# Kernel optimization log

Measured on AMD Instinct MI355X. Metric: run time of the kernel, lower is better.

Reference implementation:

```python
import jax, jax.numpy as jnp
import numpy as np
from jax import lax

B, T, DE, DT = 64, 511, 400, 100
D = DE + DT              # encoder + tag embedding concat
S = T + 1                # head sentinel prepended
HG, HE, M = 384, 64, 32  # graph hidden, edge hidden, band width


def lstm_layer(x, h0, c0, Wih, Whh, bih, bhh):
    """x: [N, L, in] -> [N, L, H]; torch LSTM gate order (i, f, g, o)."""
    def step(carry, xt):
        h, c = carry
        gates = xt @ Wih.T + bih + h @ Whh.T + bhh
        i, f, g, o = jnp.split(gates, 4, axis=-1)
        c = jax.nn.sigmoid(f) * c + jax.nn.sigmoid(i) * jnp.tanh(g)
        h = jax.nn.sigmoid(o) * jnp.tanh(c)
        return (h, c), h
    _, ys = lax.scan(step, (h0, c0), jnp.swapaxes(x, 0, 1))
    return jnp.swapaxes(ys, 0, 1)


def setup_inputs() -> dict:
    key = jax.random.key(0)
    ks = jax.random.split(key, 32)
    def u(k, shape, h):
        s = 1.0 / np.sqrt(h)
        return jax.random.uniform(k, shape, jnp.float32, -s, s)
    return {
        "input": jax.random.normal(ks[0], (B, T, DE), jnp.float32),
        "tag_embeddings": jax.random.normal(ks[1], (B, T, DT), jnp.float32),
        "mask": jnp.ones((B, T), jnp.int32),
        "head_indices": jax.random.randint(ks[2], (B, T), 0, S),
        "head_sentinel": jax.random.normal(ks[3], (D,), jnp.float32),
        "bos_past": jnp.zeros((1,), jnp.float32),
        # graph LSTM (2 layers, dropout inactive at eval)
        "g_Wih0": u(ks[4], (4 * HG, D), HG),  "g_Whh0": u(ks[5], (4 * HG, HG), HG),
        "g_bih0": u(ks[6], (4 * HG,), HG),     "g_bhh0": u(ks[7], (4 * HG,), HG),
        "g_Wih1": u(ks[8], (4 * HG, HG), HG),  "g_Whh1": u(ks[9], (4 * HG, HG), HG),
        "g_bih1": u(ks[10], (4 * HG,), HG),    "g_bhh1": u(ks[11], (4 * HG,), HG),
        # edge LSTM past (2 layers, input size 1)
        "e_Wih0": u(ks[12], (4 * HE, 1), HE),  "e_Whh0": u(ks[13], (4 * HE, HE), HE),
        "e_bih0": u(ks[14], (4 * HE,), HE),    "e_bhh0": u(ks[15], (4 * HE,), HE),
        "e_Wih1": u(ks[16], (4 * HE, HE), HE), "e_Whh1": u(ks[17], (4 * HE, HE), HE),
        "e_bih1": u(ks[18], (4 * HE,), HE),    "e_bhh1": u(ks[19], (4 * HE,), HE),
        "g2e_W": u(ks[20], (HE, HG), HG),      "g2e_b": u(ks[21], (HE,), HG),
        "cls_W": u(ks[22], (1, HE), HE),       "cls_b": u(ks[23], (1,), HE),
        "ht_W": u(ks[24], (DT, HG), HG),       "ht_b": u(ks[25], (DT,), HG),
        "dt_W": u(ks[26], (DT, HG), HG),       "dt_b": u(ks[27], (DT,), HG),
    }


def reference(input, tag_embeddings, mask, head_indices, head_sentinel, bos_past,
              g_Wih0, g_Whh0, g_bih0, g_bhh0, g_Wih1, g_Whh1, g_bih1, g_bhh1,
              e_Wih0, e_Whh0, e_bih0, e_bhh0, e_Wih1, e_Whh1, e_bih1, e_bhh1,
              g2e_W, g2e_b, cls_W, cls_b, ht_W, ht_b, dt_W, dt_b):
    # --- sentinel prepend + adjust_for_sentinel ---
    x = jnp.concatenate([input, tag_embeddings], axis=-1)                      # [B,T,D]
    x = jnp.concatenate([jnp.broadcast_to(head_sentinel, (B, 1, D)), x], 1)    # [B,S,D]
    mask_s = jnp.concatenate([jnp.ones((B, 1), mask.dtype), mask], axis=1)
    heads = jnp.concatenate([jnp.zeros((B, 1), head_indices.dtype), head_indices], axis=1)
    # --- packed graph LSTM (2 layers, zero init); pad_packed zeros masked positions ---
    zg = jnp.zeros((B, HG), x.dtype)
    h = lstm_layer(x, zg, zg, g_Wih0, g_Whh0, g_bih0, g_bhh0)
    graph_state = lstm_layer(h, zg, zg, g_Wih1, g_Whh1, g_bih1, g_bhh1)        # [B,S,HG]
    graph_state = graph_state * mask_s[..., None].astype(graph_state.dtype)
    # --- edge_pass_train (split=False): teacher-forced banded edge LSTM ---
    proj = graph_state.reshape(B * S, HG) @ g2e_W.T + g2e_b                    # [B*S,HE]
    Lm = min(M, S)
    A_sq = jax.nn.one_hot(heads, S, dtype=jnp.float32)                         # adj_indices_to_adj_matrix
    A_in = A_sq[:, :, :Lm].reshape(B * S, Lm, 1)                               # make_adj_sequence band
    bos = jnp.broadcast_to(bos_past.reshape(1, 1, 1), (B * S, 1, 1))
    A_in = jnp.concatenate([bos, A_in], axis=1)                                # [B*S,Lm+1,1]
    ze = jnp.zeros((B * S, HE), proj.dtype)
    e = lstm_layer(A_in, proj, ze, e_Wih0, e_Whh0, e_bih0, e_bhh0)             # h0=proj per layer, c0=0
    e = lstm_layer(e, proj, ze, e_Wih1, e_Whh1, e_bih1, e_bhh1)
    edge_logits = e @ cls_W.T + cls_b                                          # [B*S,Lm+1,1]
    Ap = edge_logits[:, 1:, 0].reshape(B, S, Lm)                               # drop bos step
    # banded writeback: arc_logits[:, i, :min(S,M)] = Ap[:, i, :] for every i
    arc_logits = jnp.zeros((B, S, S), graph_state.dtype).at[:, :, :Lm].set(Ap)
    # --- tag feedforwards (dropout = identity at eval) ---
    head_tag = jax.nn.elu(graph_state @ ht_W.T + ht_b)
    dep_tag = jax.nn.elu(graph_state @ dt_W.T + dt_b)
    return arc_logits, head_tag, dep_tag
```

## Files before the change

kernel.cpp:

```cpp
#include <hip/hip_runtime.h>
#include <hip/hip_bf16.h>
#include <stdint.h>

#define BB   64
#define TT   511
#define SS   512
#define DD   500
#define KXP  512
#define HG   384
#define G4   1536
#define HE   64
#define E4   256
#define NSEQ (BB*SS)

typedef __hip_bfloat16 bf16;
typedef float  floatx4 __attribute__((ext_vector_type(4)));
typedef int    intx4   __attribute__((ext_vector_type(4)));
typedef __bf16 bfrag8  __attribute__((ext_vector_type(8)));

static __device__ __forceinline__ floatx4 MFMA16(bfrag8 a, bfrag8 b, floatx4 c){
  return __builtin_amdgcn_mfma_f32_16x16x32_bf16(a, b, c, 0, 0, 0);
}
static __device__ __forceinline__ float sigm_(float x){ return 1.f/(1.f + __expf(-x)); }
static __device__ __forceinline__ float tanh_(float x){
  x = fminf(fmaxf(x, -15.f), 15.f);
  float e = __expf(2.f*x);
  return (e - 1.f)/(e + 1.f);
}
static __device__ __forceinline__ float actv(float x, bool isg){
  float s = 1.f/(1.f + __expf(isg ? -2.f*x : -x));
  return isg ? (2.f*s - 1.f) : s;
}
static __device__ __forceinline__ float b2f(unsigned short u){
  union { unsigned int i; float f; } x; x.i = ((unsigned int)u)<<16; return x.f;
}
static __device__ __forceinline__ unsigned short f2bu(float f){
  bf16 b = __float2bfloat16(f);
  return *reinterpret_cast<unsigned short*>(&b);
}
static __device__ __forceinline__ bfrag8 asfrag(intx4 v){
  union { intx4 i; bfrag8 f; } u; u.i = v; return u.f;
}

static __device__ __forceinline__ bfrag8 ldfrag_coh(const bf16* p){
  unsigned long long u0 = __hip_atomic_load((const unsigned long long*)p,     __ATOMIC_RELAXED, __HIP_MEMORY_SCOPE_SYSTEM);
  unsigned long long u1 = __hip_atomic_load((const unsigned long long*)p + 1, __ATOMIC_RELAXED, __HIP_MEMORY_SCOPE_SYSTEM);
  union { unsigned long long u[2]; bfrag8 f; } x; x.u[0]=u0; x.u[1]=u1;
  return x.f;
}
static __device__ __forceinline__ void stpair_coh(bf16* p, float lo, float hi){
  unsigned int pk = (unsigned int)f2bu(lo) | ((unsigned int)f2bu(hi) << 16);
  __hip_atomic_store((unsigned int*)p, pk, __ATOMIC_RELAXED, __HIP_MEMORY_SCOPE_SYSTEM);
}
static __device__ __forceinline__ void pollge(unsigned int* p, unsigned int tgt){
  while (__hip_atomic_load(p, __ATOMIC_RELAXED, __HIP_MEMORY_SCOPE_AGENT) < tgt)
    __builtin_amdgcn_s_sleep(4);
}

__global__ __launch_bounds__(256) void prep_x(const float* __restrict__ input,
    const float* __restrict__ tag, const float* __restrict__ sent,
    bf16* __restrict__ Xb)
{
  const size_t stp = (size_t)gridDim.x * blockDim.x;
  for (size_t i = (size_t)blockIdx.x*blockDim.x + threadIdx.x; i < (size_t)NSEQ*KXP; i += stp){
    int m = (int)(i >> 9), k = (int)(i & 511);
    int b = m >> 9, s = m & 511;
    float v;
    if (k >= DD)        v = 0.f;
    else if (s == 0)    v = sent[k];
    else if (k < 400)   v = input[(size_t)(b*TT + s-1)*400 + k];
    else                v = tag  [(size_t)(b*TT + s-1)*100 + (k-400)];
    Xb[i] = __float2bfloat16(v);
  }
}

__global__ __launch_bounds__(256) void prep_w(
  const float* __restrict__ gWih0, const float* __restrict__ gWhh0,
  const float* __restrict__ gbih0, const float* __restrict__ gbhh0,
  const float* __restrict__ gWih1, const float* __restrict__ gWhh1,
  const float* __restrict__ gbih1, const float* __restrict__ gbhh1,
  const float* __restrict__ eWih0, const float* __restrict__ eWhh0,
  const float* __restrict__ ebih0, const float* __restrict__ ebhh0,
  const float* __restrict__ eWih1, const float* __restrict__ eWhh1,
  const float* __restrict__ ebih1, const float* __restrict__ ebhh1,
  const float* __restrict__ g2eW, const float* __restrict__ htW, const float* __restrict__ dtW,
  bf16* __restrict__ W0i, bf16* __restrict__ W0r, bf16* __restrict__ W1c,
  float* __restrict__ gb0, float* __restrict__ gb1,
  bf16* __restrict__ eW0b, bf16* __restrict__ eW1ab, bf16* __restrict__ eW1bb,
  float* __restrict__ eb0, float* __restrict__ eb1, float* __restrict__ ew0cv,
  bf16* __restrict__ g2eWb, bf16* __restrict__ htWb, bf16* __restrict__ dtWb)
{
  const int st = blockIdx.x*blockDim.x + threadIdx.x;
  const int gs = gridDim.x*blockDim.x;
  for (int i=st; i<G4*KXP; i+=gs){ int n=i>>9, k=i&511; int j=n>>2, g=n&3;
      W0i[i] = __float2bfloat16(k<DD ? gWih0[(size_t)(g*HG+j)*DD+k] : 0.f); }
  for (int i=st; i<G4*HG; i+=gs){ int n=i/HG, k=i-n*HG; int j=n>>2, g=n&3;
      W0r[i] = __float2bfloat16(gWhh0[(size_t)(g*HG+j)*HG+k]); }
  for (int i=st; i<G4*768; i+=gs){ int n=i/768, k=i-n*768; int j=n>>2, g=n&3;
      W1c[i] = __float2bfloat16(k<HG ? gWih1[(size_t)(g*HG+j)*HG+k]
                                     : gWhh1[(size_t)(g*HG+j)*HG+(k-HG)]); }
  for (int i=st; i<G4; i+=gs){ int j=i>>2, g=i&3; int s=g*HG+j;
      gb0[i]=gbih0[s]+gbhh0[s]; gb1[i]=gbih1[s]+gbhh1[s]; }
  for (int i=st; i<E4*HE; i+=gs){ eW0b[i]=__float2bfloat16(eWhh0[i]);
      eW1ab[i]=__float2bfloat16(eWih1[i]); eW1bb[i]=__float2bfloat16(eWhh1[i]); }
  for (int i=st; i<E4; i+=gs){ eb0[i]=ebih0[i]+ebhh0[i]; eb1[i]=ebih1[i]+ebhh1[i];
      ew0cv[i]=eWih0[i]; }
  for (int i=st; i<HE*HG; i+=gs) g2eWb[i]=__float2bfloat16(g2eW[i]);
  for (int i=st; i<128*HG; i+=gs){
      htWb[i] = __float2bfloat16(i<100*HG ? htW[i] : 0.f);
      dtWb[i] = __float2bfloat16(i<100*HG ? dtW[i] : 0.f); }
}

template<int KTOT,int BN,int WAVES_M,int WAVES_N,int EPI>
__global__ __launch_bounds__(256) void gemm_mfma(
    const bf16* __restrict__ A, const bf16* __restrict__ Wt,
    const float* __restrict__ bias, const int* __restrict__ mask,
    void* __restrict__ outp, int Nreal)
{
  constexpr int WMT = 128/(WAVES_M*16);
  constexpr int WNT = BN /(WAVES_N*16);
  __shared__ alignas(16) bf16 As[128][32];
  __shared__ alignas(16) bf16 Bs[BN][32];
  const int tid = threadIdx.x;
  const int bm = blockIdx.x & 255, bn = blockIdx.x >> 8;
  const int m0 = bm*128, n0 = bn*BN;
  const int wid = tid>>6, l = tid&63, lj = l&15, lq = l>>4;
  const int wm = wid / WAVES_N, wn = wid % WAVES_N;
  floatx4 acc[WMT][WNT] = {};
  for (int k0 = 0; k0 < KTOT; k0 += 32){
    __syncthreads();
    for (int c = tid; c < 128*4; c += 256){
      int row = c>>2, ch = c&3;
      *(uint4*)&As[row][ch*8] = *(const uint4*)&A[(size_t)(m0+row)*KTOT + k0 + ch*8];
    }
    for (int c = tid; c < BN*4; c += 256){
      int row = c>>2, ch = c&3;
      *(uint4*)&Bs[row][ch*8] = *(const uint4*)&Wt[(size_t)(n0+row)*KTOT + k0 + ch*8];
    }
    __syncthreads();
    bfrag8 af[WMT]; bfrag8 bfr[WNT];
    #pragma unroll
    for (int mi=0;mi<WMT;++mi) af[mi]  = *(const bfrag8*)&As[wm*WMT*16 + mi*16 + lj][lq*8];
    #pragma unroll
    for (int ni=0;ni<WNT;++ni) bfr[ni] = *(const bfrag8*)&Bs[wn*WNT*16 + ni*16 + lj][lq*8];
    #pragma unroll
    for (int mi=0;mi<WMT;++mi)
      #pragma unroll
      for (int ni=0;ni<WNT;++ni)
        acc[mi][ni] = MFMA16(af[mi], bfr[ni], acc[mi][ni]);
  }
  #pragma unroll
  for (int mi=0;mi<WMT;++mi){
    #pragma unroll
    for (int ni=0;ni<WNT;++ni){
      #pragma unroll
      for (int r=0;r<4;++r){
        int grow = m0 + wm*WMT*16 + mi*16 + 4*lq + r;
        int gcol = n0 + wn*WNT*16 + ni*16 + lj;
        float v = acc[mi][ni][r];
        if (EPI == 0){
          v += bias[gcol];
          ((bf16*)outp)[(size_t)grow*Nreal + gcol] = __float2bfloat16(v);
        } else if (EPI == 3){
          v += bias[gcol];
          int s = grow & 511, b = grow >> 9;
          ((bf16*)outp)[((size_t)s*BB + b)*G4 + gcol] = __float2bfloat16(v);
        } else {
          int s = grow & 511, b = grow >> 9;
          float mk = (s==0) ? 1.f : (float)mask[b*TT + s - 1];
          v = v*mk + bias[gcol];
          if (EPI == 1){
            ((bf16*)outp)[(size_t)grow*Nreal + gcol] = __float2bfloat16(v);
          } else {
            v = v > 0.f ? v : expm1f(v);
            if (gcol < Nreal) ((float*)outp)[(size_t)grow*Nreal + gcol] = v;
          }
        }
      }
    }
  }
}

template<int IS1>
__device__ __forceinline__ void rnn_body(int bid, int tid,
    const bf16* __restrict__ G0t, const bf16* __restrict__ Wsrc,
    const float* __restrict__ gb1,
    bf16* __restrict__ h0r, bf16* __restrict__ h1seq, unsigned int* __restrict__ flags)
{
  constexpr int KW = IS1 ? 768 : 384;
  constexpr int KF = IS1 ? 24 : 12;
  const int bl = IS1 ? bid-48 : bid;
  const int w = tid>>6, l = tid&63, lj = l&15, lq = l>>4;
  const int m0 = w*16;
  const int n0 = bl*32;
  const int a  = lj>>2;
  const int gl = l&3;
  const bool isg = (gl==2);

  intx4 Wr0[KF], Wr1[KF];
  #pragma unroll
  for (int kf=0; kf<KF; ++kf){
    Wr0[kf] = *(const intx4*)&Wsrc[(size_t)(n0 + lj)*KW      + kf*32 + lq*8];
    Wr1[kf] = *(const intx4*)&Wsrc[(size_t)(n0 + 16 + lj)*KW + kf*32 + lq*8];
  }
  #pragma unroll
  for (int kf=0; kf<KF; ++kf)
    asm volatile("" : "+v"(Wr0[kf]), "+v"(Wr1[kf]));

  float bi0 = 0.f, bi1 = 0.f;
  if (IS1){ bi0 = gb1[n0 + 4*a + gl]; bi1 = gb1[n0 + 16 + 4*a + gl]; }

  float c0s[4]={0,0,0,0}, c1s[4]={0,0,0,0};
  unsigned short g0pre[2][4];
  if (!IS1){
    #pragma unroll
    for (int nt=0;nt<2;++nt)
      #pragma unroll
      for (int r=0;r<4;++r)
        g0pre[nt][r] = *(const unsigned short*)&G0t[(size_t)(m0 + 4*lq + r)*G4 + n0 + nt*16 + 4*a + gl];
  }
  const int ITMAX = IS1 ? SS : (SS-1);
  for (int it=0; it<=ITMAX; ++it){
    if (it > 0){
      if (tid < 48){
        pollge(&flags[(size_t)tid*16], (unsigned)it);
      } else if (tid < 96){
        if (IS1){ if (it >= 2) pollge(&flags[(size_t)tid*16], (unsigned)it); }
        else    { if (it >= 3) pollge(&flags[(size_t)tid*16], (unsigned)(it-2)); }
      }
      __syncthreads();
    }
    if (!IS1 || it >= 1){
      const int t = IS1 ? it-1 : it;
      bfrag8 ha[KF];
      if (IS1){
        const bf16* hb0 = h0r + (size_t)((it-1)&3)*(BB*HG) + (size_t)(m0+lj)*HG;
        #pragma unroll
        for (int kf=0;kf<12;++kf) ha[kf] = ldfrag_coh(hb0 + kf*32 + lq*8);
        if (t > 0){
          const bf16* hb1 = h1seq + ((size_t)(m0+lj)*SS + (t-1))*HG;
          #pragma unroll
          for (int kf=12;kf<24;++kf) ha[kf] = ldfrag_coh(hb1 + (kf-12)*32 + lq*8);
        }
      } else if (t > 0){
        const bf16* hb = h0r + (size_t)((t-1)&3)*(BB*HG) + (size_t)(m0+lj)*HG;
        #pragma unroll
        for (int kf=0;kf<12;++kf) ha[kf] = ldfrag_coh(hb + kf*32 + lq*8);
      }
      floatx4 aA0={0,0,0,0}, aB0={0,0,0,0}, aA1={0,0,0,0}, aB1={0,0,0,0};
      if (IS1 || t > 0){
        #pragma unroll
        for (int kf=0;kf<12;++kf){
          if (kf&1){ aB0 = MFMA16(ha[kf], asfrag(Wr0[kf]), aB0); aB1 = MFMA16(ha[kf], asfrag(Wr1[kf]), aB1); }
          else     { aA0 = MFMA16(ha[kf], asfrag(Wr0[kf]), aA0); aA1 = MFMA16(ha[kf], asfrag(Wr1[kf]), aA1); }
        }
      }
      if (IS1 && t > 0){
        #pragma unroll
        for (int kf=12;kf<24;++kf){
          if (kf&1){ aB0 = MFMA16(ha[kf], asfrag(Wr0[kf]), aB0); aB1 = MFMA16(ha[kf], asfrag(Wr1[kf]), aB1); }
          else     { aA0 = MFMA16(ha[kf], asfrag(Wr0[kf]), aA0); aA1 = MFMA16(ha[kf], asfrag(Wr1[kf]), aA1); }
        }
      }
      const floatx4 s0 = aA0 + aB0, s1 = aA1 + aB1;
      #pragma unroll
      for (int nt=0; nt<2; ++nt){
        #pragma unroll
        for (int r=0; r<4; ++r){
          float x = nt ? s1[r] : s0[r];
          x += IS1 ? (nt ? bi1 : bi0) : b2f(g0pre[nt][r]);
          float av = actv(x, isg);
          float i_ = __shfl(av, (l&60)|0);
          float f_ = __shfl(av, (l&60)|1);
          float g_ = __shfl(av, (l&60)|2);
          float o_ = __shfl(av, (l&60)|3);
          float cp = nt ? c1s[r] : c0s[r];
          float c = f_*cp + i_*g_;
          if (nt) c1s[r] = c; else c0s[r] = c;
          float h = o_*tanh_(c);
          float hn = __shfl(h, l^4);
          if ((l&7) == 0){
            int bb = m0 + 4*lq + r;
            int jh = bl*8 + nt*4 + a;
            bf16* hp = IS1 ? (h1seq + ((size_t)bb*SS + t)*HG + jh)
                           : (h0r + (size_t)(it&3)*(BB*HG) + (size_t)bb*HG + jh);
            stpair_coh(hp, h, hn);
          }
        }
      }
      if (!IS1 && it+1 < SS){
        #pragma unroll
        for (int nt=0;nt<2;++nt)
          #pragma unroll
          for (int r=0;r<4;++r)
            g0pre[nt][r] = *(const unsigned short*)&G0t[((size_t)(it+1)*BB + m0 + 4*lq + r)*G4 + n0 + nt*16 + 4*a + gl];
      }
    }
    asm volatile("s_waitcnt vmcnt(0) lgkmcnt(0)" ::: "memory");
    __syncthreads();
    if (tid == 0)
      __hip_atomic_store(&flags[(size_t)bid*16], (unsigned)(it+1),
                         __ATOMIC_RELAXED, __HIP_MEMORY_SCOPE_AGENT);
  }
}

__global__ __launch_bounds__(256,1) void graph_rnn(
    const bf16* __restrict__ G0t, const bf16* __restrict__ W0r, const bf16* __restrict__ W1c,
    const float* __restrict__ gb1, bf16* __restrict__ h0r, bf16* __restrict__ h1seq,
    unsigned int* flags)
{
  if (blockIdx.x < 48) rnn_body<0>(blockIdx.x, threadIdx.x, G0t, W0r, gb1, h0r, h1seq, flags);
  else                 rnn_body<1>(blockIdx.x, threadIdx.x, G0t, W1c, gb1, h0r, h1seq, flags);
}

__global__ __launch_bounds__(256) void edge_lstm(
    const bf16* __restrict__ projb,
    const bf16* __restrict__ eW0b, const bf16* __restrict__ eW1ab, const bf16* __restrict__ eW1bb,
    const float* __restrict__ eb0, const float* __restrict__ eb1, const float* __restrict__ ew0c,
    const float* __restrict__ clsW, const float* __restrict__ clsb_p, const float* __restrict__ bos_p,
    const int* __restrict__ heads, float* __restrict__ arc)
{
  __shared__ alignas(16) bf16 hbuf0[16][72];
  __shared__ alignas(16) bf16 hbuf1[16][72];
  __shared__ float lbuf[4][16];
  const int tid = threadIdx.x, w = tid>>6, l = tid&63, lj = l&15, lq = l>>4;
  const int seq0 = blockIdx.x * 16;
  const int jglob = w*16 + lj;
  for (int i = tid; i < 16*64; i += 256){
    int sl = i >> 6, jj = i & 63;
    bf16 v = projb[(size_t)(seq0+sl)*HE + jj];
    hbuf0[sl][jj] = v; hbuf1[sl][jj] = v;
  }
  bfrag8 W0f[4][2], W1af[4][2], W1bf[4][2];
  #pragma unroll
  for (int g=0; g<4; ++g){
    #pragma unroll
    for (int kk=0; kk<2; ++kk){
      size_t offw = (size_t)(g*HE + jglob)*HE + kk*32 + lq*8;
      W0f [g][kk] = *(const bfrag8*)&eW0b [offw];
      W1af[g][kk] = *(const bfrag8*)&eW1ab[offw];
      W1bf[g][kk] = *(const bfrag8*)&eW1bb[offw];
    }
  }
  float ebr0[4], ebr1[4], ewr[4];
  #pragma unroll
  for (int g=0; g<4; ++g){ ebr0[g]=eb0[g*HE+jglob]; ebr1[g]=eb1[g*HE+jglob]; ewr[g]=ew0c[g*HE+jglob]; }
  const float clswj = clsW[jglob];
  const float bos = bos_p[0], clsb = clsb_p[0];
  int hd[4]; float c0r[4]={0,0,0,0}, c1r[4]={0,0,0,0};
  #pragma unroll
  for (int r=0;r<4;++r){
    int sq = seq0 + 4*lq + r;
    int b = sq >> 9, s = sq & 511;
    hd[r] = (s==0) ? 0 : heads[b*TT + s - 1];
  }
  __syncthreads();
  for (int j=0; j<33; ++j){
    floatx4 acc0[4] = {};
    bfrag8 a0[2];
    #pragma unroll
    for (int kk=0; kk<2; ++kk)
      a0[kk] = *(const bfrag8*)((const char*)&hbuf0[0][0] + lj*144 + kk*64 + lq*16);
    #pragma unroll
    for (int g=0; g<4; ++g)
      #pragma unroll
      for (int kk=0; kk<2; ++kk)
        acc0[g] = MFMA16(a0[kk], W0f[g][kk], acc0[g]);
    __syncthreads();
    float h0v[4];
    #pragma unroll
    for (int r=0;r<4;++r){
      float x = (j==0) ? bos : ((hd[r] == j-1) ? 1.f : 0.f);
      float pi = acc0[0][r] + ebr0[0] + x*ewr[0];
      float pf = acc0[1][r] + ebr0[1] + x*ewr[1];
      float pg = acc0[2][r] + ebr0[2] + x*ewr[2];
      float po = acc0[3][r] + ebr0[3] + x*ewr[3];
      float i_=sigm_(pi), f_=sigm_(pf), g_=tanh_(pg), o_=sigm_(po);
      c0r[r] = f_*c0r[r] + i_*g_;
      h0v[r] = o_*tanh_(c0r[r]);
    }
    #pragma unroll
    for (int r=0;r<4;++r) hbuf0[4*lq + r][jglob] = __float2bfloat16(h0v[r]);
    __syncthreads();
    floatx4 acc1[4] = {};
    bfrag8 a1[2], a2[2];
    #pragma unroll
    for (int kk=0;kk<2;++kk){
      a1[kk] = *(const bfrag8*)((const char*)&hbuf0[0][0] + lj*144 + kk*64 + lq*16);
      a2[kk] = *(const bfrag8*)((const char*)&hbuf1[0][0] + lj*144 + kk*64 + lq*16);
    }
    #pragma unroll
    for (int g=0; g<4; ++g){
      #pragma unroll
      for (int kk=0;kk<2;++kk){
        acc1[g] = MFMA16(a1[kk], W1af[g][kk], acc1[g]);
        acc1[g] = MFMA16(a2[kk], W1bf[g][kk], acc1[g]);
      }
    }
    __syncthreads();
    float p[4];
    #pragma unroll
    for (int r=0;r<4;++r){
      float pi = acc1[0][r] + ebr1[0];
      float pf = acc1[1][r] + ebr1[1];
      float pg = acc1[2][r] + ebr1[2];
      float po = acc1[3][r] + ebr1[3];
      float i_=sigm_(pi), f_=sigm_(pf), g_=tanh_(pg), o_=sigm_(po);
      c1r[r] = f_*c1r[r] + i_*g_;
      float h1 = o_*tanh_(c1r[r]);
      hbuf1[4*lq + r][jglob] = __float2bfloat16(h1);
      p[r] = h1 * clswj;
    }
    #pragma unroll
    for (int mk=1; mk<16; mk<<=1)
      #pragma unroll
      for (int r=0;r<4;++r) p[r] += __shfl_xor(p[r], mk, 64);
    if (lj == 0){
      #pragma unroll
      for (int r=0;r<4;++r) lbuf[w][4*lq + r] = p[r];
    }
    __syncthreads();
    if (tid < 16 && j >= 1){
      int sq = seq0 + tid;
      float v = lbuf[0][tid] + lbuf[1][tid] + lbuf[2][tid] + lbuf[3][tid] + clsb;
      arc[(size_t)sq*SS + (j-1)] = v;
    }
  }
}

extern "C" void kernel_launch(void* const* d_in, const int* in_sizes, int n_in,
                              void* d_out, int out_size, void* d_ws, size_t ws_size,
                              hipStream_t stream)
{
  const float* input = (const float*)d_in[0];
  const float* tag   = (const float*)d_in[1];
  const int*   mask  = (const int*)  d_in[2];
  const int*   heads = (const int*)  d_in[3];
  const float* sent  = (const float*)d_in[4];
  const float* bosp  = (const float*)d_in[5];
  const float* gWih0 = (const float*)d_in[6];
  const float* gWhh0 = (const float*)d_in[7];
  const float* gbih0 = (const float*)d_in[8];
  const float* gbhh0 = (const float*)d_in[9];
  const float* gWih1 = (const float*)d_in[10];
  const float* gWhh1 = (const float*)d_in[11];
  const float* gbih1 = (const float*)d_in[12];
  const float* gbhh1 = (const float*)d_in[13];
  const float* eWih0 = (const float*)d_in[14];
  const float* eWhh0 = (const float*)d_in[15];
  const float* ebih0 = (const float*)d_in[16];
  const float* ebhh0 = (const float*)d_in[17];
  const float* eWih1 = (const float*)d_in[18];
  const float* eWhh1 = (const float*)d_in[19];
  const float* ebih1 = (const float*)d_in[20];
  const float* ebhh1 = (const float*)d_in[21];
  const float* g2eW  = (const float*)d_in[22];
  const float* g2eb  = (const float*)d_in[23];
  const float* clsW  = (const float*)d_in[24];
  const float* clsb  = (const float*)d_in[25];
  const float* htW   = (const float*)d_in[26];
  const float* htb   = (const float*)d_in[27];
  const float* dtW   = (const float*)d_in[28];
  const float* dtb   = (const float*)d_in[29];

  char* wsb = (char*)d_ws;
  size_t off = 0;
  auto take = [&](size_t bytes)->char* {
    char* p = wsb + off;
    off = (off + bytes + 255) & ~(size_t)255;
    return p;
  };
  bf16*  Xb     = (bf16*) take((size_t)NSEQ*KXP*2);
  bf16*  W0i    = (bf16*) take((size_t)G4*KXP*2);
  bf16*  W0r    = (bf16*) take((size_t)G4*HG*2);
  bf16*  W1c    = (bf16*) take((size_t)G4*768*2);
  float* gb0i   = (float*)take(G4*4);
  float* gb1i   = (float*)take(G4*4);
  bf16*  G0t    = (bf16*) take((size_t)NSEQ*G4*2);
  bf16*  h0ring = (bf16*) take((size_t)4*BB*HG*2);
  bf16*  h1seq  = (bf16*) take((size_t)NSEQ*HG*2);
  unsigned int* flags = (unsigned int*)take(96*16*4);
  bf16*  projb  = (bf16*) take((size_t)NSEQ*HE*2);
  bf16*  eW0b   = (bf16*) take(E4*HE*2);
  bf16*  eW1ab  = (bf16*) take(E4*HE*2);
  bf16*  eW1bb  = (bf16*) take(E4*HE*2);
  float* eb0w   = (float*)take(E4*4);
  float* eb1w   = (float*)take(E4*4);
  float* ew0cw  = (float*)take(E4*4);
  bf16*  g2eWb  = (bf16*) take(HE*HG*2);
  bf16*  htWb   = (bf16*) take(128*HG*2);
  bf16*  dtWb   = (bf16*) take(128*HG*2);

  (void)hipMemsetAsync(d_out, 0, (size_t)16777216*4, stream);
  (void)hipMemsetAsync(flags, 0, 96*16*4, stream);

  prep_x<<<2048,256,0,stream>>>(input, tag, sent, Xb);
  prep_w<<<512,256,0,stream>>>(gWih0,gWhh0,gbih0,gbhh0,gWih1,gWhh1,gbih1,gbhh1,
                               eWih0,eWhh0,ebih0,ebhh0,eWih1,eWhh1,ebih1,ebhh1,
                               g2eW,htW,dtW,
                               W0i,W0r,W1c,gb0i,gb1i,eW0b,eW1ab,eW1bb,
                               eb0w,eb1w,ew0cw,g2eWb,htWb,dtWb);

  gemm_mfma<KXP,128,2,2,3><<<3072,256,0,stream>>>(Xb, W0i, gb0i, nullptr, (void*)G0t, G4);

  graph_rnn<<<96,256,0,stream>>>(G0t, W0r, W1c, gb1i, h0ring, h1seq, flags);

  gemm_mfma<HG,64,4,1,1><<<256,256,0,stream>>>(h1seq, g2eWb, g2eb, mask, (void*)projb, HE);

  edge_lstm<<<2048,256,0,stream>>>(projb, eW0b, eW1ab, eW1bb, eb0w, eb1w, ew0cw,
                                   clsW, clsb, bosp, heads, (float*)d_out);

  gemm_mfma<HG,128,2,2,2><<<256,256,0,stream>>>(h1seq, htWb, htb, mask,
      (void*)((float*)d_out + 16777216), 100);
  gemm_mfma<HG,128,2,2,2><<<256,256,0,stream>>>(h1seq, dtWb, dtb, mask,
      (void*)((float*)d_out + 16777216 + 3276800), 100);
}
```

Baseline: 4.934 ms.

## Replace per-step flag barriers with poison-sentinel dataflow sync in graph RNN

```diff
diff --git a/kernel.cpp b/kernel.cpp
--- a/kernel.cpp
+++ b/kernel.cpp
@@ -12,6 +12,8 @@
 #define HE   64
 #define E4   256
 #define NSEQ (BB*SS)
+#define NRING 32
+#define POISON32 0x7FC07FC0u
 
 typedef __hip_bfloat16 bf16;
 typedef float  floatx4 __attribute__((ext_vector_type(4)));
@@ -42,19 +44,22 @@
   union { intx4 i; bfrag8 f; } u; u.i = v; return u.f;
 }
 
-static __device__ __forceinline__ bfrag8 ldfrag_coh(const bf16* p){
+static __device__ __forceinline__ intx4 ld16_chk(const bf16* p){
   unsigned long long u0 = __hip_atomic_load((const unsigned long long*)p,     __ATOMIC_RELAXED, __HIP_MEMORY_SCOPE_SYSTEM);
   unsigned long long u1 = __hip_atomic_load((const unsigned long long*)p + 1, __ATOMIC_RELAXED, __HIP_MEMORY_SCOPE_SYSTEM);
-  union { unsigned long long u[2]; bfrag8 f; } x; x.u[0]=u0; x.u[1]=u1;
-  return x.f;
+  union { unsigned long long u[2]; intx4 v; } x; x.u[0]=u0; x.u[1]=u1;
+  return x.v;
+}
+static __device__ __forceinline__ bool okfrag(intx4 v){
+  return (((unsigned)v.x) != POISON32) & (((unsigned)v.y) != POISON32) &
+         (((unsigned)v.z) != POISON32) & (((unsigned)v.w) != POISON32);
 }
 static __device__ __forceinline__ void stpair_coh(bf16* p, float lo, float hi){
   unsigned int pk = (unsigned int)f2bu(lo) | ((unsigned int)f2bu(hi) << 16);
   __hip_atomic_store((unsigned int*)p, pk, __ATOMIC_RELAXED, __HIP_MEMORY_SCOPE_SYSTEM);
 }
-static __device__ __forceinline__ void pollge(unsigned int* p, unsigned int tgt){
-  while (__hip_atomic_load(p, __ATOMIC_RELAXED, __HIP_MEMORY_SCOPE_AGENT) < tgt)
-    __builtin_amdgcn_s_sleep(4);
+static __device__ __forceinline__ void st_poison(bf16* p){
+  __hip_atomic_store((unsigned int*)p, POISON32, __ATOMIC_RELAXED, __HIP_MEMORY_SCOPE_SYSTEM);
 }
 
 __global__ __launch_bounds__(256) void prep_x(const float* __restrict__ input,
@@ -88,7 +93,8 @@
   float* __restrict__ gb0, float* __restrict__ gb1,
   bf16* __restrict__ eW0b, bf16* __restrict__ eW1ab, bf16* __restrict__ eW1bb,
   float* __restrict__ eb0, float* __restrict__ eb1, float* __restrict__ ew0cv,
-  bf16* __restrict__ g2eWb, bf16* __restrict__ htWb, bf16* __restrict__ dtWb)
+  bf16* __restrict__ g2eWb, bf16* __restrict__ htWb, bf16* __restrict__ dtWb,
+  unsigned int* __restrict__ ring_u, unsigned int* __restrict__ h1_u)
 {
   const int st = blockIdx.x*blockDim.x + threadIdx.x;
   const int gs = gridDim.x*blockDim.x;
@@ -109,6 +115,8 @@
   for (int i=st; i<128*HG; i+=gs){
       htWb[i] = __float2bfloat16(i<100*HG ? htW[i] : 0.f);
       dtWb[i] = __float2bfloat16(i<100*HG ? dtW[i] : 0.f); }
+  for (int i=st; i<NRING*BB*HG/2; i+=gs) ring_u[i] = POISON32;
+  for (int i=st; i<NSEQ*HG/2;     i+=gs) h1_u[i]   = POISON32;
 }
 
 template<int KTOT,int BN,int WAVES_M,int WAVES_N,int EPI>
@@ -221,45 +229,64 @@
   }
   const int ITMAX = IS1 ? SS : (SS-1);
   for (int it=0; it<=ITMAX; ++it){
-    if (it > 0){
-      if (tid < 48){
-        pollge(&flags[(size_t)tid*16], (unsigned)it);
-      } else if (tid < 96){
-        if (IS1){ if (it >= 2) pollge(&flags[(size_t)tid*16], (unsigned)it); }
-        else    { if (it >= 3) pollge(&flags[(size_t)tid*16], (unsigned)(it-2)); }
-      }
-      __syncthreads();
+    if (!IS1 && (it&7)==0 && it>=16){
+      const unsigned tgt = (unsigned)(it-8);
+      while (true){
+        unsigned f0 = __hip_atomic_load(&flags[(size_t)(l)*16],     __ATOMIC_RELAXED, __HIP_MEMORY_SCOPE_AGENT);
+        unsigned f1 = __hip_atomic_load(&flags[(size_t)(l+64)*16],  __ATOMIC_RELAXED, __HIP_MEMORY_SCOPE_AGENT);
+        unsigned f2 = __hip_atomic_load(&flags[(size_t)(l+128)*16], __ATOMIC_RELAXED, __HIP_MEMORY_SCOPE_AGENT);
+        if (__all(f0>=tgt && f1>=tgt && f2>=tgt)) break;
+        __builtin_amdgcn_s_sleep(16);
+      }
     }
     if (!IS1 || it >= 1){
       const int t = IS1 ? it-1 : it;
-      bfrag8 ha[KF];
+      intx4 ha[KF];
       if (IS1){
-        const bf16* hb0 = h0r + (size_t)((it-1)&3)*(BB*HG) + (size_t)(m0+lj)*HG;
-        #pragma unroll
-        for (int kf=0;kf<12;++kf) ha[kf] = ldfrag_coh(hb0 + kf*32 + lq*8);
+        const bf16* hb0 = h0r + (size_t)((it-1)&(NRING-1))*(BB*HG) + (size_t)(m0+lj)*HG;
         if (t > 0){
           const bf16* hb1 = h1seq + ((size_t)(m0+lj)*SS + (t-1))*HG;
-          #pragma unroll
-          for (int kf=12;kf<24;++kf) ha[kf] = ldfrag_coh(hb1 + (kf-12)*32 + lq*8);
+          while (true){
+            bool ok = true;
+            #pragma unroll
+            for (int kf=0;kf<12;++kf){ ha[kf] = ld16_chk(hb0 + kf*32 + lq*8); ok &= okfrag(ha[kf]); }
+            #pragma unroll
+            for (int kf=12;kf<24;++kf){ ha[kf] = ld16_chk(hb1 + (kf-12)*32 + lq*8); ok &= okfrag(ha[kf]); }
+            if (__all(ok)) break;
+            __builtin_amdgcn_s_sleep(1);
+          }
+        } else {
+          while (true){
+            bool ok = true;
+            #pragma unroll
+            for (int kf=0;kf<12;++kf){ ha[kf] = ld16_chk(hb0 + kf*32 + lq*8); ok &= okfrag(ha[kf]); }
+            if (__all(ok)) break;
+            __builtin_amdgcn_s_sleep(1);
+          }
         }
       } else if (t > 0){
-        const bf16* hb = h0r + (size_t)((t-1)&3)*(BB*HG) + (size_t)(m0+lj)*HG;
-        #pragma unroll
-        for (int kf=0;kf<12;++kf) ha[kf] = ldfrag_coh(hb + kf*32 + lq*8);
+        const bf16* hb = h0r + (size_t)((t-1)&(NRING-1))*(BB*HG) + (size_t)(m0+lj)*HG;
+        while (true){
+          bool ok = true;
+          #pragma unroll
+          for (int kf=0;kf<12;++kf){ ha[kf] = ld16_chk(hb + kf*32 + lq*8); ok &= okfrag(ha[kf]); }
+          if (__all(ok)) break;
+          __builtin_amdgcn_s_sleep(1);
+        }
       }
       floatx4 aA0={0,0,0,0}, aB0={0,0,0,0}, aA1={0,0,0,0}, aB1={0,0,0,0};
       if (IS1 || t > 0){
         #pragma unroll
         for (int kf=0;kf<12;++kf){
-          if (kf&1){ aB0 = MFMA16(ha[kf], asfrag(Wr0[kf]), aB0); aB1 = MFMA16(ha[kf], asfrag(Wr1[kf]), aB1); }
-          else     { aA0 = MFMA16(ha[kf], asfrag(Wr0[kf]), aA0); aA1 = MFMA16(ha[kf], asfrag(Wr1[kf]), aA1); }
+          if (kf&1){ aB0 = MFMA16(asfrag(ha[kf]), asfrag(Wr0[kf]), aB0); aB1 = MFMA16(asfrag(ha[kf]), asfrag(Wr1[kf]), aB1); }
+          else     { aA0 = MFMA16(asfrag(ha[kf]), asfrag(Wr0[kf]), aA0); aA1 = MFMA16(asfrag(ha[kf]), asfrag(Wr1[kf]), aA1); }
         }
       }
       if (IS1 && t > 0){
         #pragma unroll
         for (int kf=12;kf<24;++kf){
-          if (kf&1){ aB0 = MFMA16(ha[kf], asfrag(Wr0[kf]), aB0); aB1 = MFMA16(ha[kf], asfrag(Wr1[kf]), aB1); }
-          else     { aA0 = MFMA16(ha[kf], asfrag(Wr0[kf]), aA0); aA1 = MFMA16(ha[kf], asfrag(Wr1[kf]), aA1); }
+          if (kf&1){ aB0 = MFMA16(asfrag(ha[kf]), asfrag(Wr0[kf]), aB0); aB1 = MFMA16(asfrag(ha[kf]), asfrag(Wr1[kf]), aB1); }
+          else     { aA0 = MFMA16(asfrag(ha[kf]), asfrag(Wr0[kf]), aA0); aA1 = MFMA16(asfrag(ha[kf]), asfrag(Wr1[kf]), aA1); }
         }
       }
       const floatx4 s0 = aA0 + aB0, s1 = aA1 + aB1;
@@ -283,10 +310,21 @@
             int bb = m0 + 4*lq + r;
             int jh = bl*8 + nt*4 + a;
             bf16* hp = IS1 ? (h1seq + ((size_t)bb*SS + t)*HG + jh)
-                           : (h0r + (size_t)(it&3)*(BB*HG) + (size_t)bb*HG + jh);
+                           : (h0r + (size_t)(it&(NRING-1))*(BB*HG) + (size_t)bb*HG + jh);
             stpair_coh(hp, h, hn);
           }
         }
+      }
+      if (!IS1 && (l&7) == 0){
+        bf16* ps = h0r + (size_t)((it+8)&(NRING-1))*(BB*HG);
+        #pragma unroll
+        for (int nt=0;nt<2;++nt)
+          #pragma unroll
+          for (int r=0;r<4;++r){
+            int bb = m0 + 4*lq + r;
+            int jh = bl*8 + nt*4 + a;
+            st_poison(ps + (size_t)bb*HG + jh);
+          }
       }
       if (!IS1 && it+1 < SS){
         #pragma unroll
@@ -296,10 +334,8 @@
             g0pre[nt][r] = *(const unsigned short*)&G0t[((size_t)(it+1)*BB + m0 + 4*lq + r)*G4 + n0 + nt*16 + 4*a + gl];
       }
     }
-    asm volatile("s_waitcnt vmcnt(0) lgkmcnt(0)" ::: "memory");
-    __syncthreads();
-    if (tid == 0)
-      __hip_atomic_store(&flags[(size_t)bid*16], (unsigned)(it+1),
+    if (IS1 && l == 0)
+      __hip_atomic_store(&flags[(size_t)(bl*4 + w)*16], (unsigned)(it+1),
                          __ATOMIC_RELAXED, __HIP_MEMORY_SCOPE_AGENT);
   }
 }
@@ -477,9 +513,9 @@
   float* gb0i   = (float*)take(G4*4);
   float* gb1i   = (float*)take(G4*4);
   bf16*  G0t    = (bf16*) take((size_t)NSEQ*G4*2);
-  bf16*  h0ring = (bf16*) take((size_t)4*BB*HG*2);
+  bf16*  h0ring = (bf16*) take((size_t)NRING*BB*HG*2);
   bf16*  h1seq  = (bf16*) take((size_t)NSEQ*HG*2);
-  unsigned int* flags = (unsigned int*)take(96*16*4);
+  unsigned int* flags = (unsigned int*)take(192*16*4);
   bf16*  projb  = (bf16*) take((size_t)NSEQ*HE*2);
   bf16*  eW0b   = (bf16*) take(E4*HE*2);
   bf16*  eW1ab  = (bf16*) take(E4*HE*2);
@@ -492,14 +528,15 @@
   bf16*  dtWb   = (bf16*) take(128*HG*2);
 
   (void)hipMemsetAsync(d_out, 0, (size_t)16777216*4, stream);
-  (void)hipMemsetAsync(flags, 0, 96*16*4, stream);
+  (void)hipMemsetAsync(flags, 0, 192*16*4, stream);
 
   prep_x<<<2048,256,0,stream>>>(input, tag, sent, Xb);
   prep_w<<<512,256,0,stream>>>(gWih0,gWhh0,gbih0,gbhh0,gWih1,gWhh1,gbih1,gbhh1,
                                eWih0,eWhh0,ebih0,ebhh0,eWih1,eWhh1,ebih1,ebhh1,
                                g2eW,htW,dtW,
                                W0i,W0r,W1c,gb0i,gb1i,eW0b,eW1ab,eW1bb,
-                               eb0w,eb1w,ew0cw,g2eWb,htWb,dtWb);
+                               eb0w,eb1w,ew0cw,g2eWb,htWb,dtWb,
+                               (unsigned int*)h0ring, (unsigned int*)h1seq);
 
   gemm_mfma<KXP,128,2,2,3><<<3072,256,0,stream>>>(Xb, W0i, gb0i, nullptr, (void*)G0t, G4);
 
```

Result: slower. 7.380 ms (+49.6%).

## Replace block-level barriers with per-wave flags in persistent graph LSTM

Applied to the files above, without the earlier changes.

```diff
diff --git a/kernel.cpp b/kernel.cpp
--- a/kernel.cpp
+++ b/kernel.cpp
@@ -51,10 +51,6 @@
 static __device__ __forceinline__ void stpair_coh(bf16* p, float lo, float hi){
   unsigned int pk = (unsigned int)f2bu(lo) | ((unsigned int)f2bu(hi) << 16);
   __hip_atomic_store((unsigned int*)p, pk, __ATOMIC_RELAXED, __HIP_MEMORY_SCOPE_SYSTEM);
-}
-static __device__ __forceinline__ void pollge(unsigned int* p, unsigned int tgt){
-  while (__hip_atomic_load(p, __ATOMIC_RELAXED, __HIP_MEMORY_SCOPE_AGENT) < tgt)
-    __builtin_amdgcn_s_sleep(4);
 }
 
 __global__ __launch_bounds__(256) void prep_x(const float* __restrict__ input,
@@ -185,7 +181,7 @@
 __device__ __forceinline__ void rnn_body(int bid, int tid,
     const bf16* __restrict__ G0t, const bf16* __restrict__ Wsrc,
     const float* __restrict__ gb1,
-    bf16* __restrict__ h0r, bf16* __restrict__ h1seq, unsigned int* __restrict__ flags)
+    bf16* __restrict__ h0seq, bf16* __restrict__ h1seq, unsigned int* __restrict__ flags)
 {
   constexpr int KW = IS1 ? 768 : 384;
   constexpr int KF = IS1 ? 24 : 12;
@@ -219,22 +215,35 @@
       for (int r=0;r<4;++r)
         g0pre[nt][r] = *(const unsigned short*)&G0t[(size_t)(m0 + 4*lq + r)*G4 + n0 + nt*16 + 4*a + gl];
   }
+  unsigned int* myflag = flags + (size_t)(((IS1?48:0) + bl)*4 + w)*16;
+  unsigned int* f0p = flags + (size_t)((l)*4 + w)*16;
+  unsigned int* f1p = flags + (size_t)((48 + l)*4 + w)*16;
+
   const int ITMAX = IS1 ? SS : (SS-1);
   for (int it=0; it<=ITMAX; ++it){
-    if (it > 0){
-      if (tid < 48){
-        pollge(&flags[(size_t)tid*16], (unsigned)it);
-      } else if (tid < 96){
-        if (IS1){ if (it >= 2) pollge(&flags[(size_t)tid*16], (unsigned)it); }
-        else    { if (it >= 3) pollge(&flags[(size_t)tid*16], (unsigned)(it-2)); }
-      }
-      __syncthreads();
+    if (it >= 1){
+      const unsigned tgt = (unsigned)it;
+      const bool need = (l < 48);
+      while (true){
+        bool ok = true;
+        if (need){
+          unsigned f0 = __hip_atomic_load(f0p, __ATOMIC_RELAXED, __HIP_MEMORY_SCOPE_AGENT);
+          ok = (f0 >= tgt);
+          if (IS1){
+            unsigned f1 = __hip_atomic_load(f1p, __ATOMIC_RELAXED, __HIP_MEMORY_SCOPE_AGENT);
+            ok = ok && (f1 >= tgt);
+          }
+        }
+        if (__all(ok)) break;
+        __builtin_amdgcn_s_sleep(1);
+      }
+      asm volatile("" ::: "memory");
     }
     if (!IS1 || it >= 1){
       const int t = IS1 ? it-1 : it;
       bfrag8 ha[KF];
       if (IS1){
-        const bf16* hb0 = h0r + (size_t)((it-1)&3)*(BB*HG) + (size_t)(m0+lj)*HG;
+        const bf16* hb0 = h0seq + ((size_t)t*BB + (m0+lj))*HG;
         #pragma unroll
         for (int kf=0;kf<12;++kf) ha[kf] = ldfrag_coh(hb0 + kf*32 + lq*8);
         if (t > 0){
@@ -243,7 +252,7 @@
           for (int kf=12;kf<24;++kf) ha[kf] = ldfrag_coh(hb1 + (kf-12)*32 + lq*8);
         }
       } else if (t > 0){
-        const bf16* hb = h0r + (size_t)((t-1)&3)*(BB*HG) + (size_t)(m0+lj)*HG;
+        const bf16* hb = h0seq + ((size_t)(t-1)*BB + (m0+lj))*HG;
         #pragma unroll
         for (int kf=0;kf<12;++kf) ha[kf] = ldfrag_coh(hb + kf*32 + lq*8);
       }
@@ -283,34 +292,33 @@
             int bb = m0 + 4*lq + r;
             int jh = bl*8 + nt*4 + a;
             bf16* hp = IS1 ? (h1seq + ((size_t)bb*SS + t)*HG + jh)
-                           : (h0r + (size_t)(it&3)*(BB*HG) + (size_t)bb*HG + jh);
+                           : (h0seq + ((size_t)t*BB + bb)*HG + jh);
             stpair_coh(hp, h, hn);
           }
         }
       }
-      if (!IS1 && it+1 < SS){
+    }
+    asm volatile("s_waitcnt vmcnt(0)" ::: "memory");
+    if (l == 0)
+      __hip_atomic_store(myflag, (unsigned)(it+1),
+                         __ATOMIC_RELAXED, __HIP_MEMORY_SCOPE_AGENT);
+    if (!IS1 && it+1 <= ITMAX){
+      #pragma unroll
+      for (int nt=0;nt<2;++nt)
         #pragma unroll
-        for (int nt=0;nt<2;++nt)
-          #pragma unroll
-          for (int r=0;r<4;++r)
-            g0pre[nt][r] = *(const unsigned short*)&G0t[((size_t)(it+1)*BB + m0 + 4*lq + r)*G4 + n0 + nt*16 + 4*a + gl];
-      }
-    }
-    asm volatile("s_waitcnt vmcnt(0) lgkmcnt(0)" ::: "memory");
-    __syncthreads();
-    if (tid == 0)
-      __hip_atomic_store(&flags[(size_t)bid*16], (unsigned)(it+1),
-                         __ATOMIC_RELAXED, __HIP_MEMORY_SCOPE_AGENT);
+        for (int r=0;r<4;++r)
+          g0pre[nt][r] = *(const unsigned short*)&G0t[((size_t)(it+1)*BB + m0 + 4*lq + r)*G4 + n0 + nt*16 + 4*a + gl];
+    }
   }
 }
 
 __global__ __launch_bounds__(256,1) void graph_rnn(
     const bf16* __restrict__ G0t, const bf16* __restrict__ W0r, const bf16* __restrict__ W1c,
-    const float* __restrict__ gb1, bf16* __restrict__ h0r, bf16* __restrict__ h1seq,
+    const float* __restrict__ gb1, bf16* __restrict__ h0seq, bf16* __restrict__ h1seq,
     unsigned int* flags)
 {
-  if (blockIdx.x < 48) rnn_body<0>(blockIdx.x, threadIdx.x, G0t, W0r, gb1, h0r, h1seq, flags);
-  else                 rnn_body<1>(blockIdx.x, threadIdx.x, G0t, W1c, gb1, h0r, h1seq, flags);
+  if (blockIdx.x < 48) rnn_body<0>(blockIdx.x, threadIdx.x, G0t, W0r, gb1, h0seq, h1seq, flags);
+  else                 rnn_body<1>(blockIdx.x, threadIdx.x, G0t, W1c, gb1, h0seq, h1seq, flags);
 }
 
 __global__ __launch_bounds__(256) void edge_lstm(
@@ -477,9 +485,9 @@
   float* gb0i   = (float*)take(G4*4);
   float* gb1i   = (float*)take(G4*4);
   bf16*  G0t    = (bf16*) take((size_t)NSEQ*G4*2);
-  bf16*  h0ring = (bf16*) take((size_t)4*BB*HG*2);
+  bf16*  h0seq  = (bf16*) take((size_t)SS*BB*HG*2);
   bf16*  h1seq  = (bf16*) take((size_t)NSEQ*HG*2);
-  unsigned int* flags = (unsigned int*)take(96*16*4);
+  unsigned int* flags = (unsigned int*)take(384*16*4);
   bf16*  projb  = (bf16*) take((size_t)NSEQ*HE*2);
   bf16*  eW0b   = (bf16*) take(E4*HE*2);
   bf16*  eW1ab  = (bf16*) take(E4*HE*2);
@@ -492,7 +500,7 @@
   bf16*  dtWb   = (bf16*) take(128*HG*2);
 
   (void)hipMemsetAsync(d_out, 0, (size_t)16777216*4, stream);
-  (void)hipMemsetAsync(flags, 0, 96*16*4, stream);
+  (void)hipMemsetAsync(flags, 0, 384*16*4, stream);
 
   prep_x<<<2048,256,0,stream>>>(input, tag, sent, Xb);
   prep_w<<<512,256,0,stream>>>(gWih0,gWhh0,gbih0,gbhh0,gWih1,gWhh1,gbih1,gbhh1,
@@ -503,7 +511,7 @@
 
   gemm_mfma<KXP,128,2,2,3><<<3072,256,0,stream>>>(Xb, W0i, gb0i, nullptr, (void*)G0t, G4);
 
-  graph_rnn<<<96,256,0,stream>>>(G0t, W0r, W1c, gb1i, h0ring, h1seq, flags);
+  graph_rnn<<<96,256,0,stream>>>(G0t, W0r, W1c, gb1i, h0seq, h1seq, flags);
 
   gemm_mfma<HG,64,4,1,1><<<256,256,0,stream>>>(h1seq, g2eWb, g2eb, mask, (void*)projb, HE);
 
```

After: 4.936 ms. About the same (+0.1%).
